# Performance work log

Measured on AMD Instinct MI355X. Metric: run time of the kernel, lower is better.

## Reference

```python
import jax, jax.numpy as jnp
import numpy as np

N_SAMPLE = 256
POS_IOU_THRESH = 0.7
NEG_IOU_THRESH = 0.3
POS_RATIO = 0.5


def _bbox_iou(bbox_a, bbox_b):
    # bbox_a: [K,4], bbox_b: [G,4] in (x1,y1,x2,y2)
    tl = jnp.maximum(bbox_a[:, None, :2], bbox_b[None, :, :2])  # [K,G,2]
    br = jnp.minimum(bbox_a[:, None, 2:], bbox_b[None, :, 2:])  # [K,G,2]
    wh = br - tl
    inter = wh[..., 0] * wh[..., 1] * jnp.all(tl < br, axis=2)  # [K,G]
    area_a = (bbox_a[:, 2] - bbox_a[:, 0]) * (bbox_a[:, 3] - bbox_a[:, 1])
    area_b = (bbox_b[:, 2] - bbox_b[:, 0]) * (bbox_b[:, 3] - bbox_b[:, 1])
    return inter / (area_a[:, None] + area_b[None, :] - inter)


def _bbox2loc(src_bbox, dst_bbox):
    eps = jnp.asarray(np.finfo(np.float32).eps, src_bbox.dtype)
    width = jnp.maximum(src_bbox[:, 2] - src_bbox[:, 0], eps)
    height = jnp.maximum(src_bbox[:, 3] - src_bbox[:, 1], eps)
    ctr_x = src_bbox[:, 0] + 0.5 * (src_bbox[:, 2] - src_bbox[:, 0])
    ctr_y = src_bbox[:, 1] + 0.5 * (src_bbox[:, 3] - src_bbox[:, 1])
    base_w = dst_bbox[:, 2] - dst_bbox[:, 0]
    base_h = dst_bbox[:, 3] - dst_bbox[:, 1]
    base_cx = dst_bbox[:, 0] + 0.5 * base_w
    base_cy = dst_bbox[:, 1] + 0.5 * base_h
    dx = (base_cx - ctr_x) / width
    dy = (base_cy - ctr_y) / height
    dw = jnp.log(base_w / width)
    dh = jnp.log(base_h / height)
    return jnp.stack([dx, dy, dw, dh], axis=1)  # [K,4]


def _masked_rank(mask, priority):
    # rank (0-based, by priority) of each element within the masked subset;
    # elements outside the mask get ranks >= subset size.
    key = jnp.where(mask, priority, jnp.inf)
    order = jnp.argsort(key)
    n = order.shape[0]
    return jnp.zeros((n,), jnp.int32).at[order].set(jnp.arange(n, dtype=jnp.int32))


def _make_boxes(key, n, coord_max, wh_min, wh_max):
    k1, k2 = jax.random.split(key)
    xy = jax.random.uniform(k1, (n, 2), jnp.float32, 0.0, coord_max)
    wh = jax.random.uniform(k2, (n, 2), jnp.float32, wh_min, wh_max)
    return jnp.concatenate([xy, xy + wh], axis=1)  # valid x1<x2, y1<y2


def setup_inputs() -> dict:
    key = jax.random.key(0)
    ka, kb = jax.random.split(key)
    anchor = _make_boxes(ka, 131072, 800.0, 8.0, 256.0)
    bbox = _make_boxes(kb, 256, 800.0, 16.0, 300.0)
    return {"anchor": anchor, "bbox": bbox}


def reference(anchor, bbox):
    K = anchor.shape[0]
    G = bbox.shape[0]
    ious = _bbox_iou(anchor, bbox)  # [K,G]
    argmax_ious = jnp.argmax(ious, axis=1).astype(jnp.int32)  # best gt per anchor
    max_ious = jnp.max(ious, axis=1)
    gt_argmax_ious = jnp.argmax(ious, axis=0)  # best anchor per gt, [G]
    # force each gt's best anchor to be assigned to that gt
    argmax_ious = argmax_ious.at[gt_argmax_ious].set(jnp.arange(G, dtype=jnp.int32))

    label = jnp.full((K,), -1, jnp.int32)
    label = jnp.where(max_ious < NEG_IOU_THRESH, 0, label)
    label = jnp.where(max_ious >= POS_IOU_THRESH, 1, label)
    label = label.at[gt_argmax_ious].set(1)

    # random subsampling of positives / negatives (fixed key, jit-friendly)
    skey = jax.random.key(42)
    k1, k2 = jax.random.split(skey)
    p_pos = jax.random.uniform(k1, (K,))
    p_neg = jax.random.uniform(k2, (K,))

    n_pos = int(POS_RATIO * N_SAMPLE)
    pos_mask = label == 1
    pos_rank = _masked_rank(pos_mask, p_pos)
    label = jnp.where(pos_mask & (pos_rank >= n_pos), -1, label)

    n_neg = N_SAMPLE - jnp.sum(label == 1)
    neg_mask = label == 0
    neg_rank = _masked_rank(neg_mask, p_neg)
    label = jnp.where(neg_mask & (neg_rank >= n_neg), -1, label)

    loc = _bbox2loc(anchor, bbox[argmax_ious])  # [K,4]
    has_pos = jnp.any(label > 0)
    loc = jnp.where(has_pos, loc, jnp.zeros_like(loc))
    return loc, label
```

## Files before the change

kernel.cpp:

```cpp
#include <hip/hip_runtime.h>
#include <stdint.h>

#define K_ANCH 131072
#define G_BOX  256
#define NPOS_TGT 128
#define NSAMPLE 256
#define POS_CAP 8192
#define NEG_CAP 32768

struct TF2 { uint32_t a, b; };

__host__ __device__ constexpr uint32_t rotl32(uint32_t v, int d) {
  return (v << d) | (v >> (32 - d));
}

__host__ __device__ constexpr TF2 threefry(uint32_t k0, uint32_t k1,
                                           uint32_t x0, uint32_t x1) {
  const uint32_t ks0 = k0, ks1 = k1, ks2 = k0 ^ k1 ^ 0x1BD11BDAu;
  const int R0[4] = {13, 15, 26, 6};
  const int R1[4] = {17, 29, 16, 24};
  x0 += ks0; x1 += ks1;
  for (int r = 0; r < 4; ++r) { x0 += x1; x1 = rotl32(x1, R0[r]); x1 ^= x0; }
  x0 += ks1; x1 += ks2 + 1u;
  for (int r = 0; r < 4; ++r) { x0 += x1; x1 = rotl32(x1, R1[r]); x1 ^= x0; }
  x0 += ks2; x1 += ks0 + 2u;
  for (int r = 0; r < 4; ++r) { x0 += x1; x1 = rotl32(x1, R0[r]); x1 ^= x0; }
  x0 += ks0; x1 += ks1 + 3u;
  for (int r = 0; r < 4; ++r) { x0 += x1; x1 = rotl32(x1, R1[r]); x1 ^= x0; }
  x0 += ks1; x1 += ks2 + 4u;
  for (int r = 0; r < 4; ++r) { x0 += x1; x1 = rotl32(x1, R0[r]); x1 ^= x0; }
  x0 += ks2; x1 += ks0 + 5u;
  return TF2{x0, x1};
}

constexpr TF2 KPOS = threefry(0u, 42u, 0u, 0u);
constexpr TF2 KNEG = threefry(0u, 42u, 0u, 1u);

__device__ __forceinline__ uint32_t rbits(TF2 k, uint32_t i) {
  TF2 r = threefry(k.a, k.b, 0u, i);
  return r.a ^ r.b;
}

__device__ __forceinline__ float p_from_bits(uint32_t bits) {
  uint32_t fb = 0x3f800000u | (bits >> 9);
  float f = __uint_as_float(fb) - 1.0f;
  return fmaxf(f, 0.0f);
}

__device__ __forceinline__ uint64_t prio_key(float p, uint32_t idx) {
  return ((uint64_t)__float_as_uint(p) << 32) | (uint64_t)idx;
}

template <int CTRL, int RMASK>
__device__ __forceinline__ uint32_t dpp_umax(uint32_t x) {
  uint32_t t = (uint32_t)__builtin_amdgcn_update_dpp((int)x, (int)x, CTRL, RMASK, 0xf, false);
  return x > t ? x : t;
}

struct ScalarBlk {
  unsigned long long cutoff[2];
  int B_pos, r_pos, B_neg, r_neg;
  int do_pos, do_neg, pos_kept, pad;
};

__global__ __launch_bounds__(256) void k_fused(const float4* __restrict__ anchor,
                                               const float4* __restrict__ bbox,
                                               int* __restrict__ argmax,
                                               int* __restrict__ label,
                                               unsigned long long* __restrict__ gkey_part) {
  __shared__ float4 gts[G_BOX];
  __shared__ float gab[G_BOX];
  __shared__ uint32_t xbest[256];
  __shared__ int xbidx[256];
  int tid = threadIdx.x;
  int al = tid & 63, q = tid >> 6;
  int abase = blockIdx.x * 64;
  int i = abase + al;

  float4 bb = bbox[tid];
  gts[tid] = bb;
  {
    #pragma clang fp contract(off)
    gab[tid] = (bb.z - bb.x) * (bb.w - bb.y);
  }
  __syncthreads();

  float4 a = anchor[i];
  float area_a;
  {
    #pragma clang fp contract(off)
    area_a = (a.z - a.x) * (a.w - a.y);
  }
  uint32_t bestbits = 0u; int bidx = 0;
  int gbase = q * 64;
  uint32_t keyhi = 0u, keylo = 0u;

  #pragma unroll 8
  for (int s = 0; s < 64; ++s) {
    int g = gbase + s;
    float4 b = gts[g];
    float ab = gab[g];
    uint32_t vb;
    {
      #pragma clang fp contract(off)
      float tlx = fmaxf(a.x, b.x), tly = fmaxf(a.y, b.y);
      float brx = fminf(a.z, b.z), bry = fminf(a.w, b.w);
      float w = brx - tlx, h = bry - tly;
      float wh = w * h;
      bool ok = (tlx < brx) && (tly < bry);
      float inter = ok ? wh : 0.0f;
      float u = (area_a + ab) - inter;
      float v = inter / u;
      vb = __float_as_uint(v);
    }
    if (vb > bestbits) { bestbits = vb; bidx = g; }
    uint32_t x = vb;
    x = dpp_umax<0x111, 0xf>(x);
    x = dpp_umax<0x112, 0xf>(x);
    x = dpp_umax<0x114, 0xf>(x);
    x = dpp_umax<0x118, 0xf>(x);
    x = dpp_umax<0x142, 0xa>(x);
    x = dpp_umax<0x143, 0xc>(x);
    uint32_t m = (uint32_t)__builtin_amdgcn_readlane((int)x, 63);
    unsigned long long ball = __ballot(vb == m);
    int lane = __ffsll((long long)ball) - 1;
    uint32_t klo = ~(uint32_t)(abase + lane);
    bool mine = (al == s);
    keyhi = mine ? m : keyhi;
    keylo = mine ? klo : keylo;
  }

  {
    unsigned long long key = ((unsigned long long)keyhi << 32) | (unsigned long long)keylo;
    atomicMax(&gkey_part[(blockIdx.x & 7) * G_BOX + gbase + al], key);
  }

  xbest[tid] = bestbits; xbidx[tid] = bidx;
  __syncthreads();
  if (tid < 64) {
    #pragma unroll
    for (int qq = 1; qq < 4; ++qq) {
      uint32_t ob = xbest[qq * 64 + tid]; int og = xbidx[qq * 64 + tid];
      if (ob > bestbits) { bestbits = ob; bidx = og; }
    }
    argmax[i] = bidx;
    float best = __uint_as_float(bestbits);
    int lbl = -1;
    if (best < 0.3f) lbl = 0;
    if (best >= 0.7f) lbl = 1;
    label[i] = lbl;
  }
}

__global__ void k_force(const unsigned long long* __restrict__ gkey_part,
                        int* __restrict__ argmax, int* __restrict__ label) {
  __shared__ int ga[G_BOX];
  int tid = threadIdx.x;
  unsigned long long best = gkey_part[tid];
  #pragma unroll
  for (int p = 1; p < 8; ++p) {
    unsigned long long o = gkey_part[p * G_BOX + tid];
    if (o > best) best = o;
  }
  ga[tid] = (int)(~(uint32_t)(best & 0xffffffffull));
  __syncthreads();
  label[ga[tid]] = 1;
  if (tid == 0) {
    for (int t = 0; t < G_BOX; ++t) argmax[ga[t]] = t;
  }
}

__global__ __launch_bounds__(256) void k_hist(const int* __restrict__ label,
                                              uint32_t* __restrict__ hist) {
  int i = blockIdx.x * 256 + threadIdx.x;
  int lbl = label[i];
  if (lbl < 0) return;
  TF2 k = (lbl == 1) ? KPOS : KNEG;
  float p = p_from_bits(rbits(k, (uint32_t)i));
  int b = (int)(p * 1024.0f); if (b > 1023) b = 1023;
  atomicAdd((unsigned int*)&hist[(lbl == 1 ? 0 : 1024) + b], 1u);
}

__global__ __launch_bounds__(256) void k_select(const uint32_t* __restrict__ hist,
                                                ScalarBlk* __restrict__ sc) {
  __shared__ uint32_t h[2048];
  for (int t = threadIdx.x; t < 2048; t += 256) h[t] = hist[t];
  __syncthreads();
  if (threadIdx.x != 0) return;
  uint32_t total_pos = 0, total_neg = 0;
  for (int b = 0; b < 1024; ++b) total_pos += h[b];
  for (int b = 0; b < 1024; ++b) total_neg += h[1024 + b];
  int pos_kept = total_pos < (uint32_t)NPOS_TGT ? (int)total_pos : NPOS_TGT;
  int n_neg = NSAMPLE - pos_kept;
  sc->pos_kept = pos_kept;
  if (total_pos <= (uint32_t)NPOS_TGT) {
    sc->do_pos = 0; sc->cutoff[0] = ~0ull;
  } else {
    uint32_t cum = 0; int B = 0;
    for (; B < 1024; ++B) { if (cum + h[B] > (uint32_t)NPOS_TGT) break; cum += h[B]; }
    sc->do_pos = 1; sc->B_pos = B; sc->r_pos = NPOS_TGT - (int)cum;
  }
  if (total_neg <= (uint32_t)n_neg) {
    sc->do_neg = 0; sc->cutoff[1] = ~0ull;
  } else {
    uint32_t cum = 0; int B = 0;
    for (; B < 1024; ++B) { if (cum + h[1024 + B] > (uint32_t)n_neg) break; cum += h[1024 + B]; }
    sc->do_neg = 1; sc->B_neg = B; sc->r_neg = n_neg - (int)cum;
  }
}

__global__ __launch_bounds__(256) void k_collect(const int* __restrict__ label,
                                                 uint64_t* __restrict__ pos_list,
                                                 uint64_t* __restrict__ neg_list,
                                                 uint32_t* __restrict__ counters,
                                                 const ScalarBlk* __restrict__ sc) {
  int i = blockIdx.x * 256 + threadIdx.x;
  int lbl = label[i];
  if (lbl < 0) return;
  if (lbl == 1) {
    if (!sc->do_pos) return;
    float p = p_from_bits(rbits(KPOS, (uint32_t)i));
    int b = (int)(p * 1024.0f); if (b > 1023) b = 1023;
    if (b != sc->B_pos) return;
    uint32_t slot = atomicAdd((unsigned int*)&counters[0], 1u);
    if (slot < POS_CAP) pos_list[slot] = prio_key(p, (uint32_t)i);
  } else {
    if (!sc->do_neg) return;
    float p = p_from_bits(rbits(KNEG, (uint32_t)i));
    int b = (int)(p * 1024.0f); if (b > 1023) b = 1023;
    if (b != sc->B_neg) return;
    uint32_t slot = atomicAdd((unsigned int*)&counters[1], 1u);
    if (slot < NEG_CAP) neg_list[slot] = prio_key(p, (uint32_t)i);
  }
}

__global__ __launch_bounds__(256) void k_cutoff(const uint64_t* __restrict__ pos_list,
                                                const uint64_t* __restrict__ neg_list,
                                                const uint32_t* __restrict__ counters,
                                                ScalarBlk* __restrict__ sc) {
  int cls = blockIdx.x;
  int doit = (cls == 0) ? sc->do_pos : sc->do_neg;
  if (!doit) return;
  const uint64_t* list = (cls == 0) ? pos_list : neg_list;
  int cap = (cls == 0) ? POS_CAP : NEG_CAP;
  int m = (int)counters[cls]; if (m > cap) m = cap;
  int r = (cls == 0) ? sc->r_pos : sc->r_neg;
  for (int j = threadIdx.x; j < m; j += 256) {
    uint64_t kj = list[j];
    int rank = 0;
    for (int t = 0; t < m; ++t) rank += (list[t] < kj) ? 1 : 0;
    if (rank == r) sc->cutoff[cls] = (unsigned long long)kj;
  }
}

__global__ __launch_bounds__(256) void k_final(const float4* __restrict__ anchor,
                                               const float4* __restrict__ bbox,
                                               const int* __restrict__ argmax,
                                               const int* __restrict__ label,
                                               const ScalarBlk* __restrict__ sc,
                                               float* __restrict__ out) {
  #pragma clang fp contract(off)
  int i = blockIdx.x * 256 + threadIdx.x;
  int lbl = label[i];
  if (lbl == 1) {
    float p = p_from_bits(rbits(KPOS, (uint32_t)i));
    if (prio_key(p, (uint32_t)i) >= sc->cutoff[0]) lbl = -1;
  } else if (lbl == 0) {
    float p = p_from_bits(rbits(KNEG, (uint32_t)i));
    if (prio_key(p, (uint32_t)i) >= sc->cutoff[1]) lbl = -1;
  }
  out[K_ANCH * 4 + i] = (float)lbl;

  float4 a = anchor[i];
  float4 b = bbox[argmax[i]];
  const float eps = 1.1920928955078125e-07f;
  float w  = fmaxf(a.z - a.x, eps);
  float h  = fmaxf(a.w - a.y, eps);
  float cx = a.x + 0.5f * (a.z - a.x);
  float cy = a.y + 0.5f * (a.w - a.y);
  float bw = b.z - b.x, bh = b.w - b.y;
  float bcx = b.x + 0.5f * bw, bcy = b.y + 0.5f * bh;
  float dx = (bcx - cx) / w, dy = (bcy - cy) / h;
  float dw = logf(bw / w), dh = logf(bh / h);
  float4 o;
  if (sc->pos_kept > 0) o = make_float4(dx, dy, dw, dh);
  else o = make_float4(0.f, 0.f, 0.f, 0.f);
  ((float4*)out)[i] = o;
}

extern "C" void kernel_launch(void* const* d_in, const int* in_sizes, int n_in,
                              void* d_out, int out_size, void* d_ws, size_t ws_size,
                              hipStream_t stream) {
  const float4* anchor = (const float4*)d_in[0];
  const float4* bbox   = (const float4*)d_in[1];
  char* ws = (char*)d_ws;

  uint32_t* hist     = (uint32_t*)(ws);
  uint32_t* counters = (uint32_t*)(ws + 8192);
  unsigned long long* gkey_part = (unsigned long long*)(ws + 16384);
  ScalarBlk* sc      = (ScalarBlk*)(ws + 32768);
  int* argmax        = (int*)(ws + 65536);
  int* label         = (int*)(ws + 65536 + 524288);
  uint64_t* pos_list = (uint64_t*)(ws + 65536 + 1048576);
  uint64_t* neg_list = pos_list + POS_CAP;

  (void)hipMemsetAsync(ws, 0, 32768, stream);
  k_fused  <<<2048, 256, 0, stream>>>(anchor, bbox, argmax, label, gkey_part);
  k_force  <<<1,    256, 0, stream>>>(gkey_part, argmax, label);
  k_hist   <<<512,  256, 0, stream>>>(label, hist);
  k_select <<<1,    256, 0, stream>>>(hist, sc);
  k_collect<<<512,  256, 0, stream>>>(label, pos_list, neg_list, counters, sc);
  k_cutoff <<<2,    256, 0, stream>>>(pos_list, neg_list, counters, sc);
  k_final  <<<512,  256, 0, stream>>>(anchor, bbox, argmax, label, sc, (float*)d_out);
}
```

Before: 143.0 us.

## Replace per-gt wave DPP reductions with shared-memory IoU tile column argmax

```diff
diff --git a/kernel.cpp b/kernel.cpp
--- a/kernel.cpp
+++ b/kernel.cpp
@@ -7,6 +7,7 @@
 #define NSAMPLE 256
 #define POS_CAP 8192
 #define NEG_CAP 32768
+#define NPART 16
 
 struct TF2 { uint32_t a, b; };
 
@@ -51,10 +52,17 @@
   return ((uint64_t)__float_as_uint(p) << 32) | (uint64_t)idx;
 }
 
-template <int CTRL, int RMASK>
-__device__ __forceinline__ uint32_t dpp_umax(uint32_t x) {
-  uint32_t t = (uint32_t)__builtin_amdgcn_update_dpp((int)x, (int)x, CTRL, RMASK, 0xf, false);
-  return x > t ? x : t;
+__device__ __forceinline__ uint32_t iou_bits(float4 a, float area_a, float4 b, float ab) {
+  #pragma clang fp contract(off)
+  float tlx = fmaxf(a.x, b.x), tly = fmaxf(a.y, b.y);
+  float brx = fminf(a.z, b.z), bry = fminf(a.w, b.w);
+  float w = brx - tlx, h = bry - tly;
+  float wh = w * h;
+  bool ok = (tlx < brx) && (tly < bry);
+  float inter = ok ? wh : 0.0f;
+  float u = (area_a + ab) - inter;
+  float v = inter / u;
+  return __float_as_uint(v);
 }
 
 struct ScalarBlk {
@@ -70,18 +78,19 @@
                                                unsigned long long* __restrict__ gkey_part) {
   __shared__ float4 gts[G_BOX];
   __shared__ float gab[G_BOX];
-  __shared__ uint32_t xbest[256];
-  __shared__ int xbidx[256];
+  __shared__ uint32_t ioum[128 * 65];
+  __shared__ uint32_t xb[4][64];
+  __shared__ int xi[4][64];
   int tid = threadIdx.x;
   int al = tid & 63, q = tid >> 6;
   int abase = blockIdx.x * 64;
   int i = abase + al;
 
-  float4 bb = bbox[tid];
-  gts[tid] = bb;
+  float4 bbv = bbox[tid];
+  gts[tid] = bbv;
   {
     #pragma clang fp contract(off)
-    gab[tid] = (bb.z - bb.x) * (bb.w - bb.y);
+    gab[tid] = (bbv.z - bbv.x) * (bbv.w - bbv.y);
   }
   __syncthreads();
 
@@ -92,59 +101,48 @@
     area_a = (a.z - a.x) * (a.w - a.y);
   }
   uint32_t bestbits = 0u; int bidx = 0;
-  int gbase = q * 64;
-  uint32_t keyhi = 0u, keylo = 0u;
-
-  #pragma unroll 8
-  for (int s = 0; s < 64; ++s) {
-    int g = gbase + s;
-    float4 b = gts[g];
-    float ab = gab[g];
-    uint32_t vb;
-    {
-      #pragma clang fp contract(off)
-      float tlx = fmaxf(a.x, b.x), tly = fmaxf(a.y, b.y);
-      float brx = fminf(a.z, b.z), bry = fminf(a.w, b.w);
-      float w = brx - tlx, h = bry - tly;
-      float wh = w * h;
-      bool ok = (tlx < brx) && (tly < bry);
-      float inter = ok ? wh : 0.0f;
-      float u = (area_a + ab) - inter;
-      float v = inter / u;
-      vb = __float_as_uint(v);
+
+  #pragma unroll
+  for (int h = 0; h < 2; ++h) {
+    int hg = h * 128;
+    #pragma unroll 8
+    for (int s = 0; s < 32; ++s) {
+      int c = q * 32 + s;
+      int g = hg + c;
+      float4 b = gts[g];
+      float ab = gab[g];
+      uint32_t vb = iou_bits(a, area_a, b, ab);
+      if (vb > bestbits) { bestbits = vb; bidx = g; }
+      ioum[c * 65 + al] = vb;
     }
-    if (vb > bestbits) { bestbits = vb; bidx = g; }
-    uint32_t x = vb;
-    x = dpp_umax<0x111, 0xf>(x);
-    x = dpp_umax<0x112, 0xf>(x);
-    x = dpp_umax<0x114, 0xf>(x);
-    x = dpp_umax<0x118, 0xf>(x);
-    x = dpp_umax<0x142, 0xa>(x);
-    x = dpp_umax<0x143, 0xc>(x);
-    uint32_t m = (uint32_t)__builtin_amdgcn_readlane((int)x, 63);
-    unsigned long long ball = __ballot(vb == m);
-    int lane = __ffsll((long long)ball) - 1;
-    uint32_t klo = ~(uint32_t)(abase + lane);
-    bool mine = (al == s);
-    keyhi = mine ? m : keyhi;
-    keylo = mine ? klo : keylo;
-  }
-
-  {
-    unsigned long long key = ((unsigned long long)keyhi << 32) | (unsigned long long)keylo;
-    atomicMax(&gkey_part[(blockIdx.x & 7) * G_BOX + gbase + al], key);
-  }
-
-  xbest[tid] = bestbits; xbidx[tid] = bidx;
+    __syncthreads();
+    if (tid < 128) {
+      int c = tid;
+      uint32_t cb = ioum[c * 65 + 0]; int ca = 0;
+      #pragma unroll 8
+      for (int aa = 1; aa < 64; ++aa) {
+        uint32_t v = ioum[c * 65 + aa];
+        if (v > cb) { cb = v; ca = aa; }
+      }
+      unsigned long long key =
+          ((unsigned long long)cb << 32) |
+          (unsigned long long)(~(uint32_t)(abase + ca));
+      atomicMax(&gkey_part[(blockIdx.x & (NPART - 1)) * G_BOX + hg + c], key);
+    }
+    __syncthreads();
+  }
+
+  xb[q][al] = bestbits; xi[q][al] = bidx;
   __syncthreads();
   if (tid < 64) {
+    uint32_t bestb = xb[0][tid]; int bi = xi[0][tid];
     #pragma unroll
     for (int qq = 1; qq < 4; ++qq) {
-      uint32_t ob = xbest[qq * 64 + tid]; int og = xbidx[qq * 64 + tid];
-      if (ob > bestbits) { bestbits = ob; bidx = og; }
+      uint32_t ob = xb[qq][tid]; int og = xi[qq][tid];
+      if (ob > bestb || (ob == bestb && og < bi)) { bestb = ob; bi = og; }
     }
-    argmax[i] = bidx;
-    float best = __uint_as_float(bestbits);
+    argmax[i] = bi;
+    float best = __uint_as_float(bestb);
     int lbl = -1;
     if (best < 0.3f) lbl = 0;
     if (best >= 0.7f) lbl = 1;
@@ -158,7 +156,7 @@
   int tid = threadIdx.x;
   unsigned long long best = gkey_part[tid];
   #pragma unroll
-  for (int p = 1; p < 8; ++p) {
+  for (int p = 1; p < NPART; ++p) {
     unsigned long long o = gkey_part[p * G_BOX + tid];
     if (o > best) best = o;
   }
@@ -298,13 +296,13 @@
   uint32_t* hist     = (uint32_t*)(ws);
   uint32_t* counters = (uint32_t*)(ws + 8192);
   unsigned long long* gkey_part = (unsigned long long*)(ws + 16384);
-  ScalarBlk* sc      = (ScalarBlk*)(ws + 32768);
+  ScalarBlk* sc      = (ScalarBlk*)(ws + 49152);
   int* argmax        = (int*)(ws + 65536);
   int* label         = (int*)(ws + 65536 + 524288);
   uint64_t* pos_list = (uint64_t*)(ws + 65536 + 1048576);
   uint64_t* neg_list = pos_list + POS_CAP;
 
-  (void)hipMemsetAsync(ws, 0, 32768, stream);
+  (void)hipMemsetAsync(ws, 0, 49152, stream);
   k_fused  <<<2048, 256, 0, stream>>>(anchor, bbox, argmax, label, gkey_part);
   k_force  <<<1,    256, 0, stream>>>(gkey_part, argmax, label);
   k_hist   <<<512,  256, 0, stream>>>(label, hist);
```

Result: faster. 129.7 us (-9.3%).
